# Performance work log

Measured on AMD Instinct MI355X. Metric: run time of the kernel, lower is better.

The kernel has to match this reference:

```python
import jax, jax.numpy as jnp
import numpy as np
from jax import lax

K_SIZE = 5  # dilated_kernel_size


def dcls_kernel(w, p, k=K_SIZE):
    """Build dense (Cout,Cin,k,k) kernel from DCLS v1 bilinear interpolation.
    w: (Cout,Cin,Kc) weights; p: (2,Cout,Cin,Kc) learnable positions."""
    lim = k // 2
    pos = jnp.clip(p, -lim, lim) + lim          # in [0, k-1]
    i = jnp.floor(pos).astype(jnp.int32)
    r = pos - i                                  # bilinear fractions
    Co, Ci, Kc = w.shape
    co = jnp.arange(Co)[:, None, None]
    ci = jnp.arange(Ci)[None, :, None]
    i1, i2 = i[0], i[1]
    r1, r2 = r[0], r[1]
    # scatter into (k+1)x(k+1) grid so i+1 never goes out of bounds, then trim
    K = jnp.zeros((Co, Ci, k + 1, k + 1), w.dtype)
    K = K.at[co, ci, i1,     i2    ].add(w * (1 - r1) * (1 - r2))
    K = K.at[co, ci, i1 + 1, i2    ].add(w * r1 * (1 - r2))
    K = K.at[co, ci, i1,     i2 + 1].add(w * (1 - r1) * r2)
    K = K.at[co, ci, i1 + 1, i2 + 1].add(w * r1 * r2)
    return K[:, :, :k, :k]


def conv2d(x, K, pad):
    return lax.conv_general_dilated(
        x, K, window_strides=(1, 1), padding=[(pad, pad), (pad, pad)],
        dimension_numbers=('NCHW', 'OIHW', 'NCHW'))


def maxpool2(x):
    return lax.reduce_window(x, -jnp.inf, lax.max, (1, 1, 2, 2), (1, 1, 2, 2), 'VALID')


def setup_inputs() -> dict:
    key = jax.random.key(0)
    ks = jax.random.split(key, 12)
    lim = K_SIZE // 2
    B = 4096
    x = jax.random.normal(ks[0], (B, 1, 28, 28), jnp.float32)
    w1 = jax.random.normal(ks[1], (32, 1, 16), jnp.float32) * 0.2
    p1 = jax.random.uniform(ks[2], (2, 32, 1, 16), jnp.float32, -lim, lim)
    b1 = jnp.zeros((32,), jnp.float32)
    w2 = jax.random.normal(ks[3], (64, 32, 32), jnp.float32) * 0.05
    p2 = jax.random.uniform(ks[4], (2, 64, 32, 32), jnp.float32, -lim, lim)
    b2 = jnp.zeros((64,), jnp.float32)
    fc1_w = jax.random.normal(ks[5], (128, 64 * 7 * 7), jnp.float32) * 0.02
    fc1_b = jnp.zeros((128,), jnp.float32)
    fc2_w = jax.random.normal(ks[6], (10, 128), jnp.float32) * 0.08
    fc2_b = jnp.zeros((10,), jnp.float32)
    return dict(x=x, w1=w1, p1=p1, b1=b1, w2=w2, p2=p2, b2=b2,
                fc1_w=fc1_w, fc1_b=fc1_b, fc2_w=fc2_w, fc2_b=fc2_b)


def reference(x, w1, p1, b1, w2, p2, b2, fc1_w, fc1_b, fc2_w, fc2_b):
    h = conv2d(x, dcls_kernel(w1, p1), pad=2) + b1[None, :, None, None]
    h = maxpool2(jax.nn.relu(h))                       # (B,32,14,14)
    h = conv2d(h, dcls_kernel(w2, p2), pad=2) + b2[None, :, None, None]
    h = maxpool2(jax.nn.relu(h))                       # (B,64,7,7)
    h = h.reshape(-1, 64 * 7 * 7)
    h = jax.nn.relu(h @ fc1_w.T + fc1_b)
    return h @ fc2_w.T + fc2_b                         # (B,10)
```

## Files before the change

kernel.cpp:

```cpp
#include <hip/hip_runtime.h>
#include <hip/hip_bf16.h>

typedef __attribute__((ext_vector_type(8))) short short8;
typedef __attribute__((ext_vector_type(4))) short short4v;
typedef __attribute__((ext_vector_type(4))) float float4v;
typedef __attribute__((ext_vector_type(16))) float float16v;

static __device__ __forceinline__ unsigned short f2bf(float f) {
    unsigned u = __float_as_uint(f);
    unsigned r = (u + 0x7FFF + ((u >> 16) & 1)) >> 16;
    return (unsigned short)r;
}

__global__ __launch_bounds__(256) void prep_all(
    const float* __restrict__ w1, const float* __restrict__ p1,
    const float* __restrict__ w2, const float* __restrict__ p2,
    const float* __restrict__ fc1w,
    unsigned short* __restrict__ K1b,
    unsigned short* __restrict__ Kt,
    unsigned short* __restrict__ w1b) {
    const int blk = blockIdx.x;
    const int t = threadIdx.x;

    if (blk < 8) {
        int cell = blk * 256 + t;
        int co = cell >> 6;
        int k = cell & 63;
        int wr = k >> 3;
        int kx = k & 7;
        float acc = 0.f;
        if (wr < 5 && kx < 5) {
#pragma unroll 8
            for (int kc = 0; kc < 16; ++kc) {
                float wv = w1[co * 16 + kc];
                float pa = p1[co * 16 + kc];
                float pb = p1[512 + co * 16 + kc];
                float pos1 = fminf(fmaxf(pa, -2.f), 2.f) + 2.f;
                float pos2 = fminf(fmaxf(pb, -2.f), 2.f) + 2.f;
                int i1 = (int)floorf(pos1);
                int i2 = (int)floorf(pos2);
                float r1 = pos1 - (float)i1;
                float r2 = pos2 - (float)i2;
                float c = 0.f;
                if (i1 == wr && i2 == kx) c += (1.f - r1) * (1.f - r2);
                if (i1 + 1 == wr && i2 == kx) c += r1 * (1.f - r2);
                if (i1 == wr && i2 + 1 == kx) c += (1.f - r1) * r2;
                if (i1 + 1 == wr && i2 + 1 == kx) c += r1 * r2;
                acc += wv * c;
            }
        }
        K1b[cell] = f2bf(acc);
    } else if (blk < 208) {
        int cell = (blk - 8) * 256 + t;
        int kk = cell >> 11;
        int co = (cell >> 5) & 63;
        int ci = cell & 31;
        int ky = kk / 5;
        int kx = kk - 5 * ky;
        const int base = (co * 32 + ci) * 32;
        float acc = 0.f;
#pragma unroll 8
        for (int kc = 0; kc < 32; ++kc) {
            float wv = w2[base + kc];
            float pa = p2[base + kc];
            float pb = p2[65536 + base + kc];
            float pos1 = fminf(fmaxf(pa, -2.f), 2.f) + 2.f;
            float pos2 = fminf(fmaxf(pb, -2.f), 2.f) + 2.f;
            int i1 = (int)floorf(pos1);
            int i2 = (int)floorf(pos2);
            float r1 = pos1 - (float)i1;
            float r2 = pos2 - (float)i2;
            float c = 0.f;
            if (i1 == ky && i2 == kx) c += (1.f - r1) * (1.f - r2);
            if (i1 + 1 == ky && i2 == kx) c += r1 * (1.f - r2);
            if (i1 == ky && i2 + 1 == kx) c += (1.f - r1) * r2;
            if (i1 + 1 == ky && i2 + 1 == kx) c += r1 * r2;
            acc += wv * c;
        }
        Kt[cell] = f2bf(acc);
    } else {
        int i8 = ((blk - 208) * 256 + t) * 8;
        float4 v0 = *(const float4*)(fc1w + i8);
        float4 v1 = *(const float4*)(fc1w + i8 + 4);
        short8 o = {(short)f2bf(v0.x), (short)f2bf(v0.y), (short)f2bf(v0.z),
                    (short)f2bf(v0.w), (short)f2bf(v1.x), (short)f2bf(v1.y),
                    (short)f2bf(v1.z), (short)f2bf(v1.w)};
        *(short8*)(w1b + i8) = o;
    }
}

__global__ __launch_bounds__(256, 4) void fused_conv_mfma(
    const float* __restrict__ x,
    const unsigned short* __restrict__ K1b,
    const unsigned short* __restrict__ Kt,
    const float* __restrict__ b1,
    const float* __restrict__ b2,
    unsigned short* __restrict__ h2) {
    __shared__ __align__(16) unsigned short h1p[18 * 20 * 40];
    __shared__ __align__(16) unsigned short sm4[4 * 29 * 44];
    __shared__ __align__(16) unsigned short sm_xb[784];

    const int b = blockIdx.x;
    const int tid = threadIdx.x;
    const int lane = tid & 63;
    const int wv = tid >> 6;
    const int n16 = lane & 15;
    const int cig = lane >> 4;

    const int yi = 2 * (n16 >> 3) + ((n16 >> 1) & 1);
    const int xi = 2 * ((n16 >> 2) & 1) + (n16 & 1);
    const int pYo = cig >> 1, pXo = cig & 1;

    const int mq = lane & 31;
    const int Qx = mq >> 2;
    const int dy2 = (mq >> 1) & 1;
    const int dx2 = mq & 1;
    const int hh = lane >> 5;

    for (int t = tid; t < 1800; t += 256) ((uint4*)h1p)[t] = uint4{0, 0, 0, 0};
    {
        const float* xb = x + (size_t)b * 784;
        for (int t = tid; t < 784; t += 256) sm_xb[t] = f2bf(xb[t]);
    }
    __syncthreads();

    if (tid < 116) {
        int s = tid / 29;
        int r = tid - s * 29;
        unsigned short* dst = sm4 + (s * 29 + r) * 44;
        bool rok = r < 28;
#pragma unroll
        for (int g = 0; g < 11; ++g) {
            short4v v;
#pragma unroll
            for (int e = 0; e < 4; ++e) {
                int c = g * 4 + e + s - 4;
                v[e] = (short)((rok && (unsigned)c < 28u) ? sm_xb[r * 28 + c]
                                                          : (unsigned short)0);
            }
            *(short4v*)(dst + g * 4) = v;
        }
    }

    short8 bw[2][2];
    float bias1[2], bias2n[2];
#pragma unroll
    for (int cot = 0; cot < 2; ++cot) {
#pragma unroll
        for (int h = 0; h < 2; ++h)
            bw[cot][h] = *(const short8*)(K1b + (cot * 16 + n16) * 64 + h * 32 + cig * 8);
        bias1[cot] = b1[cot * 16 + n16];
    }
#pragma unroll
    for (int nt = 0; nt < 2; ++nt) bias2n[nt] = b2[nt * 32 + mq];

    const int s1 = (xi + 2) & 3;
    const int pb1 = (xi + 2) & ~3;
    const unsigned short* a1base = sm4 + s1 * (29 * 44) + pb1;

    __syncthreads();

    for (int i = 0; i < 13; ++i) {
        int t = wv + 4 * i;
        if (t < 49) {
            int tY = t / 7, tX = t - 7 * tY;
            const unsigned short* ab = a1base + 4 * tX;
            int r0 = 4 * tY + yi - 2 + cig;
            int r1 = r0 + 4;
            int rr0 = ((unsigned)r0 < 28u) ? r0 : 28;
            int rr1 = ((unsigned)r1 < 28u) ? r1 : 28;
            short4v lo0 = *(const short4v*)(ab + rr0 * 44);
            short4v hi0 = *(const short4v*)(ab + rr0 * 44 + 4);
            short4v lo1 = *(const short4v*)(ab + rr1 * 44);
            short4v hi1 = *(const short4v*)(ab + rr1 * 44 + 4);
            short8 af0 = {lo0[0], lo0[1], lo0[2], lo0[3], hi0[0], hi0[1], hi0[2], hi0[3]};
            short8 af1 = {lo1[0], lo1[1], lo1[2], lo1[3], hi1[0], hi1[1], hi1[2], hi1[3]};
            int pY = 2 * tY + pYo, pX = 2 * tX + pXo;
#pragma unroll
            for (int cot = 0; cot < 2; ++cot) {
                float4v acc = {0.f, 0.f, 0.f, 0.f};
                acc = __builtin_amdgcn_mfma_f32_16x16x32_bf16(af0, bw[cot][0], acc, 0, 0, 0);
                acc = __builtin_amdgcn_mfma_f32_16x16x32_bf16(af1, bw[cot][1], acc, 0, 0, 0);
                float v = fmaxf(fmaxf(acc[0], acc[1]), fmaxf(acc[2], acc[3]));
                v = fmaxf(v + bias1[cot], 0.f);
                h1p[((pY + 2) * 20 + (pX + 2)) * 40 + cot * 16 + n16] = f2bf(v);
            }
        }
    }
    __syncthreads();

    int x2 = 2 * Qx + dx2;
    if (x2 > 13) x2 = 13;
    int aoff[2][2];
    int pYv[2];
#pragma unroll
    for (int mt = 0; mt < 2; ++mt) {
        int pY = 2 * wv + mt;
        int y2 = 2 * pY + dy2;
        if (y2 > 13) y2 = 13;
        pYv[mt] = pY;
#pragma unroll
        for (int kh2 = 0; kh2 < 2; ++kh2)
            aoff[mt][kh2] = (y2 * 20 + x2) * 40 + kh2 * 16 + hh * 8;
    }

    float16v acc2[2][2];
#pragma unroll
    for (int mt = 0; mt < 2; ++mt)
#pragma unroll
        for (int nt = 0; nt < 2; ++nt)
#pragma unroll
            for (int e = 0; e < 16; ++e) acc2[mt][nt][e] = 0.f;

#pragma unroll
    for (int ky = 0; ky < 5; ++ky) {
#pragma unroll
        for (int kx = 0; kx < 5; ++kx) {
            int kk = ky * 5 + kx;
            short8 wf[2][2];
#pragma unroll
            for (int nt = 0; nt < 2; ++nt)
#pragma unroll
                for (int kh2 = 0; kh2 < 2; ++kh2)
                    wf[nt][kh2] = *(const short8*)(Kt + kk * 2048 +
                        (nt * 32 + mq) * 32 + kh2 * 16 + hh * 8);
#pragma unroll
            for (int mt = 0; mt < 2; ++mt) {
                short8 af0 = *(const short8*)(h1p + aoff[mt][0] + (ky * 20 + kx) * 40);
                short8 af1 = *(const short8*)(h1p + aoff[mt][1] + (ky * 20 + kx) * 40);
#pragma unroll
                for (int nt = 0; nt < 2; ++nt) {
                    acc2[mt][nt] = __builtin_amdgcn_mfma_f32_32x32x16_bf16(
                        af0, wf[nt][0], acc2[mt][nt], 0, 0, 0);
                    acc2[mt][nt] = __builtin_amdgcn_mfma_f32_32x32x16_bf16(
                        af1, wf[nt][1], acc2[mt][nt], 0, 0, 0);
                }
            }
        }
    }

    unsigned short* outb = h2 + (size_t)b * 3136;
#pragma unroll
    for (int mt = 0; mt < 2; ++mt) {
        if (pYv[mt] < 7) {
#pragma unroll
            for (int nt = 0; nt < 2; ++nt) {
#pragma unroll
                for (int g = 0; g < 4; ++g) {
                    int pX = 2 * g + hh;
                    float v = fmaxf(fmaxf(acc2[mt][nt][4 * g], acc2[mt][nt][4 * g + 1]),
                                    fmaxf(acc2[mt][nt][4 * g + 2], acc2[mt][nt][4 * g + 3]));
                    v = fmaxf(v + bias2n[nt], 0.f);
                    if (pX < 7)
                        outb[(nt * 32 + mq) * 49 + pYv[mt] * 7 + pX] = f2bf(v);
                }
            }
        }
    }
}

__global__ __launch_bounds__(256) void fc1_mfma(
    const unsigned short* __restrict__ A,
    const unsigned short* __restrict__ Wb,
    float* __restrict__ part, size_t PB) {
    __shared__ __align__(16) unsigned short As[64 * 72];
    const int blk = blockIdx.x;
    const int kh = blk % 7;
    const int m0 = (blk / 7) * 64;
    const int tid = threadIdx.x;
    const int wv = tid >> 6;
    const int lane = tid & 63;
    const int n16 = lane & 15;
    const int cig = lane >> 4;

    float4v acc[4][2];
#pragma unroll
    for (int mt = 0; mt < 4; ++mt)
#pragma unroll
        for (int j = 0; j < 2; ++j) acc[mt][j] = float4v{0.f, 0.f, 0.f, 0.f};

    for (int it = 0; it < 7; ++it) {
        int k0 = kh * 448 + it * 64;
        __syncthreads();
#pragma unroll
        for (int i = 0; i < 2; ++i) {
            int p = tid + 256 * i;
            int r = p >> 3, ko = (p & 7) * 8;
            *(short8*)(As + r * 72 + ko) =
                *(const short8*)(A + (size_t)(m0 + r) * 3136 + k0 + ko);
        }
        __syncthreads();
#pragma unroll
        for (int h = 0; h < 2; ++h) {
            short8 af[4];
#pragma unroll
            for (int mt = 0; mt < 4; ++mt)
                af[mt] = *(const short8*)(As + (mt * 16 + n16) * 72 + h * 32 + cig * 8);
            short8 wf[2];
#pragma unroll
            for (int j = 0; j < 2; ++j)
                wf[j] = *(const short8*)(Wb + (size_t)((wv * 2 + j) * 16 + n16) * 3136 +
                                         k0 + h * 32 + cig * 8);
#pragma unroll
            for (int mt = 0; mt < 4; ++mt)
#pragma unroll
                for (int j = 0; j < 2; ++j)
                    acc[mt][j] = __builtin_amdgcn_mfma_f32_16x16x32_bf16(
                        af[mt], wf[j], acc[mt][j], 0, 0, 0);
        }
    }
    float* o = part + (size_t)kh * PB;
#pragma unroll
    for (int mt = 0; mt < 4; ++mt)
#pragma unroll
        for (int j = 0; j < 2; ++j)
#pragma unroll
            for (int r = 0; r < 4; ++r) {
                int row = m0 + mt * 16 + cig * 4 + r;
                o[(size_t)row * 128 + (wv * 2 + j) * 16 + n16] = acc[mt][j][r];
            }
}

__global__ __launch_bounds__(256) void fc2_kernel(
    const float* __restrict__ part, size_t PB,
    const float* __restrict__ fc1b,
    const float* __restrict__ W, const float* __restrict__ bias,
    float* __restrict__ out) {
    __shared__ float smW[10 * 132];
    __shared__ float smB1[128];
    __shared__ float smB[10];
    int t = threadIdx.x;
    for (int i = t; i < 1280; i += 256) {
        int n = i >> 7, k = i & 127;
        smW[n * 132 + k] = W[i];
    }
    if (t < 128) smB1[t] = fc1b[t];
    if (t < 10) smB[t] = bias[t];
    __syncthreads();
    const int r = t >> 3;
    const int q = t & 7;
    const size_t b = (size_t)blockIdx.x * 32 + r;
    const float* pb = part + b * 128 + q * 16;

    float rv[16];
#pragma unroll
    for (int c = 0; c < 4; ++c) {
        float4 s = *(const float4*)(pb + 4 * c);
#pragma unroll
        for (int j = 1; j < 7; ++j) {
            float4 pj = *(const float4*)(pb + (size_t)j * PB + 4 * c);
            s.x += pj.x; s.y += pj.y; s.z += pj.z; s.w += pj.w;
        }
        float4 bv = *(const float4*)(smB1 + q * 16 + 4 * c);
        rv[4 * c + 0] = fmaxf(s.x + bv.x, 0.f);
        rv[4 * c + 1] = fmaxf(s.y + bv.y, 0.f);
        rv[4 * c + 2] = fmaxf(s.z + bv.z, 0.f);
        rv[4 * c + 3] = fmaxf(s.w + bv.w, 0.f);
    }
    float acc[10];
#pragma unroll
    for (int n = 0; n < 10; ++n) {
        const float4* wr = (const float4*)(smW + n * 132 + q * 16);
        float a = 0.f;
#pragma unroll
        for (int c = 0; c < 4; ++c) {
            float4 w = wr[c];
            a += rv[4 * c] * w.x + rv[4 * c + 1] * w.y +
                 rv[4 * c + 2] * w.z + rv[4 * c + 3] * w.w;
        }
        acc[n] = a;
    }
#pragma unroll
    for (int n = 0; n < 10; ++n) {
        acc[n] += __shfl_xor(acc[n], 1);
        acc[n] += __shfl_xor(acc[n], 2);
        acc[n] += __shfl_xor(acc[n], 4);
    }
    if (q == 0) {
#pragma unroll
        for (int n = 0; n < 10; ++n) out[b * 10 + n] = acc[n] + smB[n];
    }
}

extern "C" void kernel_launch(void* const* d_in, const int* in_sizes, int n_in,
                              void* d_out, int out_size, void* d_ws, size_t ws_size,
                              hipStream_t stream) {
    const float* x    = (const float*)d_in[0];
    const float* w1   = (const float*)d_in[1];
    const float* p1   = (const float*)d_in[2];
    const float* b1   = (const float*)d_in[3];
    const float* w2   = (const float*)d_in[4];
    const float* p2   = (const float*)d_in[5];
    const float* b2   = (const float*)d_in[6];
    const float* fc1w = (const float*)d_in[7];
    const float* fc1b = (const float*)d_in[8];
    const float* fc2w = (const float*)d_in[9];
    const float* fc2b = (const float*)d_in[10];
    float* out = (float*)d_out;

    const int B = in_sizes[0] / 784;

    float* ws = (float*)d_ws;
    unsigned short* Kt  = (unsigned short*)ws;
    unsigned short* K1b = (unsigned short*)(ws + 25600);
    unsigned short* w1b = (unsigned short*)(ws + 26624);
    unsigned short* h2b = (unsigned short*)(ws + 227328);
    float* fc1p = ws + 227328 + (size_t)B * 1568;

    prep_all<<<404, 256, 0, stream>>>(w1, p1, w2, p2, fc1w, K1b, Kt, w1b);
    fused_conv_mfma<<<B, 256, 0, stream>>>(x, K1b, Kt, b1, b2, h2b);
    fc1_mfma<<<(B / 64) * 7, 256, 0, stream>>>(h2b, w1b, fc1p, (size_t)B * 128);
    fc2_kernel<<<B / 32, 256, 0, stream>>>(fc1p, (size_t)B * 128,
                                           fc1b, fc2w, fc2b, out);
}
```

Baseline: 223.2 us.

## Stage conv2 weights through double-buffered LDS, reusing conv1 scratch space

The conv2 weight slices, previously read straight from global memory by every wave, are now copied once per block into a double-buffered shared-memory tile. The copy is software-pipelined: the next tap's slice is loaded into registers while the current tap's MFMAs run, then written to the other buffer. The conv1 input scratch is aliased with the weight buffers to keep total LDS use down. This adds a __syncthreads per tap and extra LDS traffic, in exchange for fewer redundant global and L2 weight loads.

```diff
diff --git a/kernel.cpp b/kernel.cpp
--- a/kernel.cpp
+++ b/kernel.cpp
@@ -97,8 +97,11 @@
     const float* __restrict__ b2,
     unsigned short* __restrict__ h2) {
     __shared__ __align__(16) unsigned short h1p[18 * 20 * 40];
-    __shared__ __align__(16) unsigned short sm4[4 * 29 * 44];
-    __shared__ __align__(16) unsigned short sm_xb[784];
+    __shared__ __align__(16) unsigned short smu[5888];
+
+    unsigned short* sm4 = smu;
+    unsigned short* sm_xb = smu + 5104;
+    unsigned short* KtS = smu;
 
     const int b = blockIdx.x;
     const int tid = threadIdx.x;
@@ -117,6 +120,10 @@
     const int dx2 = mq & 1;
     const int hh = lane >> 5;
 
+    const int g = wv * 64 + lane;
+    const int stg_dst = (g >> 2) * 40 + (g & 3) * 8;
+    const unsigned short* stg_src = Kt + g * 8;
+
     for (int t = tid; t < 1800; t += 256) ((uint4*)h1p)[t] = uint4{0, 0, 0, 0};
     {
         const float* xb = x + (size_t)b * 784;
@@ -130,15 +137,15 @@
         unsigned short* dst = sm4 + (s * 29 + r) * 44;
         bool rok = r < 28;
 #pragma unroll
-        for (int g = 0; g < 11; ++g) {
+        for (int g2 = 0; g2 < 11; ++g2) {
             short4v v;
 #pragma unroll
             for (int e = 0; e < 4; ++e) {
-                int c = g * 4 + e + s - 4;
+                int c = g2 * 4 + e + s - 4;
                 v[e] = (short)((rok && (unsigned)c < 28u) ? sm_xb[r * 28 + c]
                                                           : (unsigned short)0);
             }
-            *(short4v*)(dst + g * 4) = v;
+            *(short4v*)(dst + g2 * 4) = v;
         }
     }
 
@@ -187,7 +194,6 @@
             }
         }
     }
-    __syncthreads();
 
     int x2 = 2 * Qx + dx2;
     if (x2 > 13) x2 = 13;
@@ -212,31 +218,49 @@
 #pragma unroll
             for (int e = 0; e < 16; ++e) acc2[mt][nt][e] = 0.f;
 
-#pragma unroll
-    for (int ky = 0; ky < 5; ++ky) {
-#pragma unroll
-        for (int kx = 0; kx < 5; ++kx) {
-            int kk = ky * 5 + kx;
-            short8 wf[2][2];
-#pragma unroll
-            for (int nt = 0; nt < 2; ++nt)
-#pragma unroll
-                for (int kh2 = 0; kh2 < 2; ++kh2)
-                    wf[nt][kh2] = *(const short8*)(Kt + kk * 2048 +
-                        (nt * 32 + mq) * 32 + kh2 * 16 + hh * 8);
-#pragma unroll
-            for (int mt = 0; mt < 2; ++mt) {
-                short8 af0 = *(const short8*)(h1p + aoff[mt][0] + (ky * 20 + kx) * 40);
-                short8 af1 = *(const short8*)(h1p + aoff[mt][1] + (ky * 20 + kx) * 40);
-#pragma unroll
-                for (int nt = 0; nt < 2; ++nt) {
-                    acc2[mt][nt] = __builtin_amdgcn_mfma_f32_32x32x16_bf16(
-                        af0, wf[nt][0], acc2[mt][nt], 0, 0, 0);
-                    acc2[mt][nt] = __builtin_amdgcn_mfma_f32_32x32x16_bf16(
-                        af1, wf[nt][1], acc2[mt][nt], 0, 0, 0);
-                }
-            }
-        }
+    const int wbase = mq * 40 + hh * 8;
+
+    short8 stg0 = *(const short8*)(stg_src);
+    __syncthreads();
+    *(short8*)(KtS + stg_dst) = stg0;
+    __syncthreads();
+
+#pragma unroll
+    for (int kk = 0; kk < 25; ++kk) {
+        const int buf = kk & 1;
+        short8 stg;
+        if (kk < 24) stg = *(const short8*)(stg_src + (kk + 1) * 2048);
+
+        const int ky = kk / 5;
+        const int kx = kk - 5 * ky;
+        const int soff = (ky * 20 + kx) * 40;
+        short8 wff[2][2], aff[2][2];
+#pragma unroll
+        for (int nt = 0; nt < 2; ++nt)
+#pragma unroll
+            for (int q = 0; q < 2; ++q)
+                wff[nt][q] = *(const short8*)(KtS + buf * 2560 + nt * 1280 +
+                                              wbase + q * 16);
+#pragma unroll
+        for (int mt = 0; mt < 2; ++mt)
+#pragma unroll
+            for (int q = 0; q < 2; ++q)
+                aff[mt][q] = *(const short8*)(h1p + aoff[mt][q] + soff);
+
+        __builtin_amdgcn_sched_barrier(0);
+#pragma unroll
+        for (int mt = 0; mt < 2; ++mt)
+#pragma unroll
+            for (int nt = 0; nt < 2; ++nt) {
+                acc2[mt][nt] = __builtin_amdgcn_mfma_f32_32x32x16_bf16(
+                    aff[mt][0], wff[nt][0], acc2[mt][nt], 0, 0, 0);
+                acc2[mt][nt] = __builtin_amdgcn_mfma_f32_32x32x16_bf16(
+                    aff[mt][1], wff[nt][1], acc2[mt][nt], 0, 0, 0);
+            }
+        __builtin_amdgcn_sched_barrier(0);
+
+        if (kk < 24) *(short8*)(KtS + (buf ^ 1) * 2560 + stg_dst) = stg;
+        __syncthreads();
     }
 
     unsigned short* outb = h2 + (size_t)b * 3136;
@@ -246,10 +270,10 @@
 #pragma unroll
             for (int nt = 0; nt < 2; ++nt) {
 #pragma unroll
-                for (int g = 0; g < 4; ++g) {
-                    int pX = 2 * g + hh;
-                    float v = fmaxf(fmaxf(acc2[mt][nt][4 * g], acc2[mt][nt][4 * g + 1]),
-                                    fmaxf(acc2[mt][nt][4 * g + 2], acc2[mt][nt][4 * g + 3]));
+                for (int g2 = 0; g2 < 4; ++g2) {
+                    int pX = 2 * g2 + hh;
+                    float v = fmaxf(fmaxf(acc2[mt][nt][4 * g2], acc2[mt][nt][4 * g2 + 1]),
+                                    fmaxf(acc2[mt][nt][4 * g2 + 2], acc2[mt][nt][4 * g2 + 3]));
                     v = fmaxf(v + bias2n[nt], 0.f);
                     if (pX < 7)
                         outb[(nt * 32 + mq) * 49 + pYv[mt] * 7 + pX] = f2bf(v);
```

Measured after the change: 209.2 us. -6.3%, faster.

## Split conv2 output channels across two 1024-thread blocks per image

Applied to the files above, without the earlier changes.

The fused conv kernel now launches two 1024-thread blocks per image. Each block computes half of the 64 conv2 output channels with 16x16x32 MFMAs, one output tile per wave. The conv2 weights are re-laid-out in the prep kernel and staged into LDS per block, and the input staging buffer is aliased into the h1 scratch to save shared memory. The aim is more parallelism and shorter per-wave dependency chains, at the cost of running conv1 twice per image, a 51 KB weight copy per block, and higher LDS use that may limit occupancy.

```diff
diff --git a/kernel.cpp b/kernel.cpp
--- a/kernel.cpp
+++ b/kernel.cpp
@@ -4,7 +4,6 @@
 typedef __attribute__((ext_vector_type(8))) short short8;
 typedef __attribute__((ext_vector_type(4))) short short4v;
 typedef __attribute__((ext_vector_type(4))) float float4v;
-typedef __attribute__((ext_vector_type(16))) float float16v;
 
 static __device__ __forceinline__ unsigned short f2bf(float f) {
     unsigned u = __float_as_uint(f);
@@ -77,7 +76,9 @@
             if (i1 + 1 == ky && i2 + 1 == kx) c += r1 * r2;
             acc += wv * c;
         }
-        Kt[cell] = f2bf(acc);
+        int cg = co >> 4, nn = co & 15;
+        int cg2 = ci >> 3, jj = ci & 7;
+        Kt[kk * 2048 + cg * 512 + cg2 * 128 + nn * 8 + jj] = f2bf(acc);
     } else {
         int i8 = ((blk - 208) * 256 + t) * 8;
         float4 v0 = *(const float4*)(fc1w + i8);
@@ -89,18 +90,19 @@
     }
 }
 
-__global__ __launch_bounds__(256, 4) void fused_conv_mfma(
+__global__ __launch_bounds__(1024, 8) void fused_conv_split(
     const float* __restrict__ x,
     const unsigned short* __restrict__ K1b,
     const unsigned short* __restrict__ Kt,
     const float* __restrict__ b1,
     const float* __restrict__ b2,
     unsigned short* __restrict__ h2) {
-    __shared__ __align__(16) unsigned short h1p[18 * 20 * 40];
-    __shared__ __align__(16) unsigned short sm4[4 * 29 * 44];
-    __shared__ __align__(16) unsigned short sm_xb[784];
-
-    const int b = blockIdx.x;
+    __shared__ __align__(16) unsigned short h1p[18 * 20 * 36];
+    __shared__ __align__(16) unsigned short KtS[25 * 1024];
+
+    const int bb = blockIdx.x;
+    const int b = bb >> 1;
+    const int chg = bb & 1;
     const int tid = threadIdx.x;
     const int lane = tid & 63;
     const int wv = tid >> 6;
@@ -111,39 +113,45 @@
     const int xi = 2 * ((n16 >> 2) & 1) + (n16 & 1);
     const int pYo = cig >> 1, pXo = cig & 1;
 
-    const int mq = lane & 31;
-    const int Qx = mq >> 2;
-    const int dy2 = (mq >> 1) & 1;
-    const int dx2 = mq & 1;
-    const int hh = lane >> 5;
-
-    for (int t = tid; t < 1800; t += 256) ((uint4*)h1p)[t] = uint4{0, 0, 0, 0};
+    const int pY = wv >> 1;
+    const int mt = wv & 1;
+    const int mrow = lane & 15;
+    const int pq = mrow >> 2, dyv = (mrow >> 1) & 1, dxv = mrow & 1;
+    int y2 = 2 * pY + dyv; if (y2 > 13) y2 = 13;
+    int x2 = 2 * (mt * 4 + pq) + dxv; if (x2 > 13) x2 = 13;
+    const int aoff = (y2 * 20 + x2) * 36 + cig * 8;
+    const int woff = lane * 8;
+
+    for (int t = tid; t < 1440; t += 1024) ((uint4*)h1p)[t] = uint4{0, 0, 0, 0};
+    if (tid < 82) ((uint4*)h1p)[1538 + tid] = uint4{0, 0, 0, 0};
     {
         const float* xb = x + (size_t)b * 784;
-        for (int t = tid; t < 784; t += 256) sm_xb[t] = f2bf(xb[t]);
-    }
-    __syncthreads();
-
+        if (tid < 784) h1p[11520 + tid] = f2bf(xb[tid]);
+    }
+    __syncthreads();
+
+    unsigned short* sm4 = KtS;
     if (tid < 116) {
         int s = tid / 29;
         int r = tid - s * 29;
         unsigned short* dst = sm4 + (s * 29 + r) * 44;
         bool rok = r < 28;
 #pragma unroll
-        for (int g = 0; g < 11; ++g) {
+        for (int g2 = 0; g2 < 11; ++g2) {
             short4v v;
 #pragma unroll
             for (int e = 0; e < 4; ++e) {
-                int c = g * 4 + e + s - 4;
-                v[e] = (short)((rok && (unsigned)c < 28u) ? sm_xb[r * 28 + c]
-                                                          : (unsigned short)0);
+                int c = g2 * 4 + e + s - 4;
+                v[e] = (short)((rok && (unsigned)c < 28u)
+                                   ? h1p[11520 + r * 28 + c]
+                                   : (unsigned short)0);
             }
-            *(short4v*)(dst + g * 4) = v;
+            *(short4v*)(dst + g2 * 4) = v;
         }
     }
 
     short8 bw[2][2];
-    float bias1[2], bias2n[2];
+    float bias1[2];
 #pragma unroll
     for (int cot = 0; cot < 2; ++cot) {
 #pragma unroll
@@ -151,8 +159,8 @@
             bw[cot][h] = *(const short8*)(K1b + (cot * 16 + n16) * 64 + h * 32 + cig * 8);
         bias1[cot] = b1[cot * 16 + n16];
     }
-#pragma unroll
-    for (int nt = 0; nt < 2; ++nt) bias2n[nt] = b2[nt * 32 + mq];
+    float bias2a = b2[chg * 32 + n16];
+    float bias2b = b2[chg * 32 + 16 + n16];
 
     const int s1 = (xi + 2) & 3;
     const int pb1 = (xi + 2) & ~3;
@@ -160,8 +168,10 @@
 
     __syncthreads();
 
-    for (int i = 0; i < 13; ++i) {
-        int t = wv + 4 * i;
+    for (int t = tid; t < 180; t += 1024) ((uint4*)h1p)[1440 + t] = uint4{0, 0, 0, 0};
+
+    for (int i = 0; i < 4; ++i) {
+        int t = wv + 16 * i;
         if (t < 49) {
             int tY = t / 7, tX = t - 7 * tY;
             const unsigned short* ab = a1base + 4 * tX;
@@ -175,7 +185,7 @@
             short4v hi1 = *(const short4v*)(ab + rr1 * 44 + 4);
             short8 af0 = {lo0[0], lo0[1], lo0[2], lo0[3], hi0[0], hi0[1], hi0[2], hi0[3]};
             short8 af1 = {lo1[0], lo1[1], lo1[2], lo1[3], hi1[0], hi1[1], hi1[2], hi1[3]};
-            int pY = 2 * tY + pYo, pX = 2 * tX + pXo;
+            int pYc = 2 * tY + pYo, pXc = 2 * tX + pXo;
 #pragma unroll
             for (int cot = 0; cot < 2; ++cot) {
                 float4v acc = {0.f, 0.f, 0.f, 0.f};
@@ -183,78 +193,52 @@
                 acc = __builtin_amdgcn_mfma_f32_16x16x32_bf16(af1, bw[cot][1], acc, 0, 0, 0);
                 float v = fmaxf(fmaxf(acc[0], acc[1]), fmaxf(acc[2], acc[3]));
                 v = fmaxf(v + bias1[cot], 0.f);
-                h1p[((pY + 2) * 20 + (pX + 2)) * 40 + cot * 16 + n16] = f2bf(v);
+                h1p[((pYc + 2) * 20 + (pXc + 2)) * 36 + cot * 16 + n16] = f2bf(v);
             }
         }
     }
     __syncthreads();
 
-    int x2 = 2 * Qx + dx2;
-    if (x2 > 13) x2 = 13;
-    int aoff[2][2];
-    int pYv[2];
-#pragma unroll
-    for (int mt = 0; mt < 2; ++mt) {
-        int pY = 2 * wv + mt;
-        int y2 = 2 * pY + dy2;
-        if (y2 > 13) y2 = 13;
-        pYv[mt] = pY;
-#pragma unroll
-        for (int kh2 = 0; kh2 < 2; ++kh2)
-            aoff[mt][kh2] = (y2 * 20 + x2) * 40 + kh2 * 16 + hh * 8;
-    }
-
-    float16v acc2[2][2];
-#pragma unroll
-    for (int mt = 0; mt < 2; ++mt)
-#pragma unroll
-        for (int nt = 0; nt < 2; ++nt)
-#pragma unroll
-            for (int e = 0; e < 16; ++e) acc2[mt][nt][e] = 0.f;
-
-#pragma unroll
+    {
+        const unsigned short* src = Kt + chg * 1024;
+        for (int g = tid; g < 3200; g += 1024) {
+            int kk = g >> 7;
+            int j = (g & 127) * 8;
+            *(short8*)(KtS + kk * 1024 + j) = *(const short8*)(src + kk * 2048 + j);
+        }
+    }
+
+    float4v acc0 = {0.f, 0.f, 0.f, 0.f};
+    float4v acc1 = {0.f, 0.f, 0.f, 0.f};
+
+    __syncthreads();
+
+    const unsigned short* afb = h1p + aoff;
+    const unsigned short* wfb = KtS + woff;
+#pragma unroll 1
     for (int ky = 0; ky < 5; ++ky) {
 #pragma unroll
         for (int kx = 0; kx < 5; ++kx) {
-            int kk = ky * 5 + kx;
-            short8 wf[2][2];
-#pragma unroll
-            for (int nt = 0; nt < 2; ++nt)
-#pragma unroll
-                for (int kh2 = 0; kh2 < 2; ++kh2)
-                    wf[nt][kh2] = *(const short8*)(Kt + kk * 2048 +
-                        (nt * 32 + mq) * 32 + kh2 * 16 + hh * 8);
-#pragma unroll
-            for (int mt = 0; mt < 2; ++mt) {
-                short8 af0 = *(const short8*)(h1p + aoff[mt][0] + (ky * 20 + kx) * 40);
-                short8 af1 = *(const short8*)(h1p + aoff[mt][1] + (ky * 20 + kx) * 40);
-#pragma unroll
-                for (int nt = 0; nt < 2; ++nt) {
-                    acc2[mt][nt] = __builtin_amdgcn_mfma_f32_32x32x16_bf16(
-                        af0, wf[nt][0], acc2[mt][nt], 0, 0, 0);
-                    acc2[mt][nt] = __builtin_amdgcn_mfma_f32_32x32x16_bf16(
-                        af1, wf[nt][1], acc2[mt][nt], 0, 0, 0);
-                }
-            }
-        }
-    }
-
-    unsigned short* outb = h2 + (size_t)b * 3136;
-#pragma unroll
-    for (int mt = 0; mt < 2; ++mt) {
-        if (pYv[mt] < 7) {
-#pragma unroll
-            for (int nt = 0; nt < 2; ++nt) {
-#pragma unroll
-                for (int g = 0; g < 4; ++g) {
-                    int pX = 2 * g + hh;
-                    float v = fmaxf(fmaxf(acc2[mt][nt][4 * g], acc2[mt][nt][4 * g + 1]),
-                                    fmaxf(acc2[mt][nt][4 * g + 2], acc2[mt][nt][4 * g + 3]));
-                    v = fmaxf(v + bias2n[nt], 0.f);
-                    if (pX < 7)
-                        outb[(nt * 32 + mq) * 49 + pYv[mt] * 7 + pX] = f2bf(v);
-                }
-            }
+            const int soff = (ky * 20 + kx) * 36;
+            const int koff = (ky * 5 + kx) * 1024;
+            short8 af = *(const short8*)(afb + soff);
+            short8 wfA = *(const short8*)(wfb + koff);
+            short8 wfB = *(const short8*)(wfb + koff + 512);
+            acc0 = __builtin_amdgcn_mfma_f32_16x16x32_bf16(af, wfA, acc0, 0, 0, 0);
+            acc1 = __builtin_amdgcn_mfma_f32_16x16x32_bf16(af, wfB, acc1, 0, 0, 0);
+        }
+    }
+
+    if (pY < 7) {
+        int pX = mt * 4 + cig;
+        if (pX < 7) {
+            unsigned short* outb = h2 + (size_t)b * 3136;
+            float v0 = fmaxf(fmaxf(acc0[0], acc0[1]), fmaxf(acc0[2], acc0[3]));
+            v0 = fmaxf(v0 + bias2a, 0.f);
+            outb[(chg * 32 + n16) * 49 + pY * 7 + pX] = f2bf(v0);
+            float v1 = fmaxf(fmaxf(acc1[0], acc1[1]), fmaxf(acc1[2], acc1[3]));
+            v1 = fmaxf(v1 + bias2b, 0.f);
+            outb[(chg * 32 + 16 + n16) * 49 + pY * 7 + pX] = f2bf(v1);
         }
     }
 }
@@ -408,7 +392,7 @@
     float* fc1p = ws + 227328 + (size_t)B * 1568;
 
     prep_all<<<404, 256, 0, stream>>>(w1, p1, w2, p2, fc1w, K1b, Kt, w1b);
-    fused_conv_mfma<<<B, 256, 0, stream>>>(x, K1b, Kt, b1, b2, h2b);
+    fused_conv_split<<<B * 2, 1024, 0, stream>>>(x, K1b, Kt, b1, b2, h2b);
     fc1_mfma<<<(B / 64) * 7, 256, 0, stream>>>(h2b, w1b, fc1p, (size_t)B * 128);
     fc2_kernel<<<B / 32, 256, 0, stream>>>(fc1p, (size_t)B * 128,
                                            fc1b, fc2w, fc2b, out);
```

Result: slower. 562.8 us (+152.1%).
